# Kernel tuning notes

Measured on AMD Instinct MI355X. Metric: run time of the kernel, lower is better.

The kernel has to match this reference:

```python
import jax, jax.numpy as jnp
import numpy as np

N, E = 65536, 524288
IN, H, OUT, L = 128, 128, 64, 2
TAU = 0.5
NUM_HEAT = 5

def _lin(x, w, b):
    return x @ w + b

def _aggregate(x, row, col, ew, n):
    # gather-mul-scatter neighbor mean: out[r] = sum_e ew[e]*x[col[e]] / max(deg[r],1)
    msg = x[col] * ew[:, None]
    out = jax.ops.segment_sum(msg, row, num_segments=n)
    deg = jnp.clip(jax.ops.segment_sum(ew, row, num_segments=n), 1.0, None)
    return out / deg[:, None]

def setup_inputs() -> dict:
    key = jax.random.key(0)
    k = jax.random.split(key, 24)
    def w(i, shape):
        fan_in = shape[-2]
        return (jax.random.normal(k[i], shape, dtype=jnp.float32) / np.sqrt(fan_in)).astype(jnp.float32)
    # every node appears in row at least once -> deg > 0 everywhere
    row = jax.random.permutation(k[0], jnp.arange(E, dtype=jnp.int32) % N)
    col = jax.random.randint(k[1], (E,), 0, N, dtype=jnp.int32)
    return {
        "x": jax.random.normal(k[2], (N, IN), dtype=jnp.float32),
        "edge_index": jnp.stack([row, col]),
        "timestamps": jax.random.uniform(k[3], (N, 1), dtype=jnp.float32),
        "edge_weight": jax.random.uniform(k[4], (E,), dtype=jnp.float32) + 0.1,
        "prev_embedding": jnp.zeros((1, H), dtype=jnp.float32),
        "gumbel": -jnp.log(-jnp.log(jax.random.uniform(k[5], (5,), minval=1e-6, maxval=1.0))),
        "ctrl_w1": w(6, (8 + H, 128)), "ctrl_b1": jnp.zeros((128,), jnp.float32),
        "ctrl_w2": w(7, (128, 5)), "ctrl_b2": jnp.zeros((5,), jnp.float32),
        "mode_bias": jnp.zeros((5,), jnp.float32),
        "att_w1": w(8, (2 * H, 64)), "att_b1": jnp.zeros((64,), jnp.float32),
        "att_w2": w(9, (64, 1)), "att_b2": jnp.zeros((1,), jnp.float32),
        "heat_kernels": jnp.linspace(0.1, 2.0, NUM_HEAT, dtype=jnp.float32),
        "tg_w": w(10, (H + 1, H)), "tg_b": jnp.zeros((H,), jnp.float32),
        "scale_weights": jnp.ones((3,), jnp.float32),
        "spatial_w": w(11, (L, H, H)), "spatial_b": jnp.zeros((L, H), jnp.float32),
        "temporal_w": w(12, (L, H, H)), "temporal_b": jnp.zeros((L, H), jnp.float32),
        "attention_w": w(13, (L, H, H)), "attention_b": jnp.zeros((L, H), jnp.float32),
        "diffusion_w": w(14, (L, H, H)), "diffusion_b": jnp.zeros((L, H), jnp.float32),
        "hier_w": w(15, (L, H, H)), "hier_b": jnp.zeros((L, H), jnp.float32),
        "out_w1": w(16, (H, H // 2)), "out_b1": jnp.zeros((H // 2,), jnp.float32),
        "out_w2": w(17, (H // 2, OUT)), "out_b2": jnp.zeros((OUT,), jnp.float32),
    }

def reference(x, edge_index, timestamps, edge_weight, prev_embedding, gumbel,
              ctrl_w1, ctrl_b1, ctrl_w2, ctrl_b2, mode_bias,
              att_w1, att_b1, att_w2, att_b2, heat_kernels, tg_w, tg_b, scale_weights,
              spatial_w, spatial_b, temporal_w, temporal_b, attention_w, attention_b,
              diffusion_w, diffusion_b, hier_w, hier_b,
              out_w1, out_b1, out_w2, out_b2):
    row, col = edge_index[0], edge_index[1]
    n, e = x.shape[0], row.shape[0]
    ones_e = jnp.ones((e,), x.dtype)
    deg = jax.ops.segment_sum(ones_e, row, num_segments=n)
    # stats are .item()-detached in torch -> stop_gradient here; torch std is unbiased (ddof=1)
    stats = jax.lax.stop_gradient(jnp.stack([
        jnp.asarray(n / 1000.0, x.dtype), jnp.asarray(e / max(n, 1), x.dtype),
        jnp.std(deg, ddof=1), (deg == 0).astype(x.dtype).mean(),
        x.mean(), jnp.std(x, ddof=1), edge_weight.mean(),
        jnp.asarray(e / (n * n), x.dtype)]))
    quality = prev_embedding.mean(axis=0)
    logits = _lin(jax.nn.relu(_lin(jnp.concatenate([stats, quality]), ctrl_w1, ctrl_b1)), ctrl_w2, ctrl_b2) + mode_bias
    probs = jax.nn.softmax((logits + gumbel) / TAU)  # soft gumbel-softmax, noise precomputed

    # spatial pass
    xs = x
    for i in range(L):
        xs = jax.nn.relu(_aggregate(_lin(xs, spatial_w[i], spatial_b[i]), row, col, edge_weight, n))
    # temporal pass
    xt = x
    for i in range(L):
        h = _lin(xt, temporal_w[i], temporal_b[i])
        gate = jax.nn.sigmoid(_lin(jnp.concatenate([h, timestamps], axis=-1), tg_w, tg_b))
        agg = _aggregate(h, row, col, ones_e, n)
        xt = jax.nn.relu(gate * h + (1 - gate) * agg)
    # attention pass (global softmax over all edges, as in torch dim=0)
    xa = x
    for i in range(L):
        h = _lin(xa, attention_w[i], attention_b[i])
        score = _lin(jax.nn.relu(_lin(jnp.concatenate([h[row], h[col]], axis=-1), att_w1, att_b1)), att_w2, att_b2)[:, 0]
        attn = jax.nn.softmax(score)
        xa = jax.nn.relu(jax.ops.segment_sum(h[col] * attn[:, None], row, num_segments=n))
    # diffusion pass
    dis = jnp.clip(deg ** -0.5, 1e-8, None)
    norm = dis[row] * dis[col]
    xd = x
    for i in range(L):
        h = _lin(xd, diffusion_w[i], diffusion_b[i])
        outs = []
        for j in range(NUM_HEAT):
            t = heat_kernels[j]
            hk = jax.ops.segment_sum(h[col] * norm[:, None], row, num_segments=n)
            h = (1 - t) * h + t * hk
            outs.append(h)
        xd = jax.nn.relu(jnp.mean(jnp.stack(outs), axis=0))
    # hierarchical pass
    xh = x
    wsc = jax.nn.softmax(scale_weights)
    for i in range(L):
        h = _lin(xh, hier_w[i], hier_b[i])
        h1 = _aggregate(h, row, col, ones_e, n)
        h2 = _aggregate(h1, row, col, ones_e, n)
        h3 = _aggregate(h2, row, col, ones_e, n)
        xh = jax.nn.relu(wsc[0] * h1 + wsc[1] * h2 + wsc[2] * h3)

    # torch skips branches with probs<=0.001 (zero contribution)
    g = jnp.where(probs > 0.001, probs, 0.0)
    xsum = g[0] * xs + g[1] * xt + g[2] * xa + g[3] * xd + g[4] * xh
    return _lin(jax.nn.relu(_lin(xsum, out_w1, out_b1)), out_w2, out_b2)
```

## Files before the change

kernel.cpp:

```cpp
#include <hip/hip_runtime.h>
#include <hip/hip_bf16.h>
#include <math.h>


#define NN   65536
#define EE   524288
#define HH   128
#define NF   (NN*HH)
#define PAD  136

typedef __hip_bfloat16 bf16;
typedef unsigned int   u32;
typedef unsigned short u16;
typedef __attribute__((ext_vector_type(8))) short s8v;
typedef __attribute__((ext_vector_type(4))) float f32x4;

__device__ __forceinline__ float b2f(bf16 v){ return __bfloat162float(v); }
__device__ __forceinline__ bf16  f2b(float v){ return __float2bfloat16(v); }
__device__ __forceinline__ float lo2f(u32 u){ return __uint_as_float(u<<16); }
__device__ __forceinline__ float hi2f(u32 u){ return __uint_as_float(u & 0xffff0000u); }
__device__ __forceinline__ u32 pack2(float a, float b){
  bf16 ba = f2b(a), bb = f2b(b);
  u16 ua = *reinterpret_cast<u16*>(&ba);
  u16 ub = *reinterpret_cast<u16*>(&bb);
  return ((u32)ub<<16) | (u32)ua;
}
__device__ __forceinline__ unsigned fenc(float f){ unsigned u=__float_as_uint(f); return (u&0x80000000u)?~u:(u|0x80000000u); }
__device__ __forceinline__ float fdec(unsigned u){ return __uint_as_float((u&0x80000000u)?(u&0x7fffffffu):~u); }
__device__ __forceinline__ float ldf(const void* p, size_t i, int isbf){
  return isbf ? b2f(((const bf16*)p)[i]) : ((const float*)p)[i];
}


__global__ void k_fill(float* p, float v, int n){
  int i = blockIdx.x*blockDim.x + threadIdx.x;
  if (i < n) p[i] = v;
}
__global__ void k_sentinel(u16* p, int n){
  int i = blockIdx.x*blockDim.x + threadIdx.x;
  if (i < n) p[i] = 0x4640;
}
__global__ void k_init(float* scal){
  int i = threadIdx.x;
  if (i < 32) scal[i] = 0.f;
  if (i == 6) ((unsigned*)scal)[6] = 0x007fffffu;
  if (i == 8) ((unsigned*)scal)[8] = 0x80000000u;
}
__global__ void k_init_attn(float* scal){
  if (threadIdx.x==0){ ((unsigned*)scal)[6] = 0x007fffffu; scal[7] = 0.f; }
}

__global__ void k_probe(const uint4* __restrict__ ew4, float* scal){
  __shared__ float red[4];
  int i = blockIdx.x*256 + threadIdx.x;
  uint4 v = ew4[i];
  float m = 0.f;
  u32 ws[4] = {v.x, v.y, v.z, v.w};
  #pragma unroll
  for (int q=0;q<4;++q){
    float a = lo2f(ws[q]), b = hi2f(ws[q]);
    a = isfinite(a) ? fabsf(a) : 1e30f;
    b = isfinite(b) ? fabsf(b) : 1e30f;
    m = fmaxf(m, fmaxf(a,b));
  }
  for (int o=32;o;o>>=1) m = fmaxf(m, __shfl_down(m, o, 64));
  if ((threadIdx.x&63)==0) red[threadIdx.x>>6] = m;
  __syncthreads();
  if (threadIdx.x==0){
    m = fmaxf(fmaxf(red[0],red[1]), fmaxf(red[2],red[3]));
    atomicMax((unsigned*)scal + 8, fenc(m));
  }
}
__global__ void k_flag(float* scal){
  if (threadIdx.x==0){
    float m = fdec(((const unsigned*)scal)[8]);
    scal[9] = (m < 64.f) ? 1.f : 0.f;
  }
}

__global__ void k_csr(const int* __restrict__ row, const int* __restrict__ col,
                      const void* __restrict__ ew, int* cnt,
                      int* __restrict__ colS, float* __restrict__ wS, const float* scal){
  int isbf = scal[9] > 0.5f;
  int e = blockIdx.x*blockDim.x + threadIdx.x;
  int r = row[e];
  float w = ldf(ew, e, isbf);
  int slot = atomicAdd(&cnt[r], 1) & 7;
  int p = r*8 + slot;
  colS[p] = col[e];
  wS[p] = w;
}

__global__ void k_node(const int* __restrict__ cnt, const float* __restrict__ wS,
                       float* deg, float* degw, float* dis, float* bsc, float* scal){
  __shared__ float red[4][4];
  int i = blockIdx.x*256 + threadIdx.x;
  float dd = (float)cnt[i];
  const float4* w4 = (const float4*)(wS + i*8);
  float4 wa = w4[0], wb = w4[1];
  float s = wa.x+wa.y+wa.z+wa.w + wb.x+wb.y+wb.z+wb.w;
  deg[i] = dd; degw[i] = s;
  dis[i] = (dd>0.f) ? (1.f/sqrtf(dd)) : 1e8f;
  bsc[i] = fminf(s, 1.f);
// ... 165 lines not shown

__global__ __launch_bounds__(256) void k_mgemm(
    const void* __restrict__ Aext, const bf16* __restrict__ Ab,
    const float* __restrict__ Af, int K,
    const bf16* __restrict__ Wt, const void* __restrict__ bias, int Boff, int Nout,
    bf16* __restrict__ outB, float* __restrict__ outF, void* __restrict__ outE,
    const void* __restrict__ ts, const float* __restrict__ rbs,
    const bf16* __restrict__ eh, const bf16* __restrict__ eg,
    int act, int bbf, const float* __restrict__ fl){
  __shared__ bf16 sA[64*PAD];
  __shared__ bf16 sW[128*PAD];
  int flA = fl[0] > 0.5f;
  int tid = threadIdx.x;
  int rowBase = blockIdx.x*64;
  {
    int tot = (Nout*PAD)/8;
    const uint4* src = (const uint4*)Wt;
    uint4* dst = (uint4*)sW;
    for (int i = tid; i < tot; i += 256) dst[i] = src[i];
  }
  {
    int kc = K/8;
    for (int i = tid; i < 64*kc; i += 256){
      int m = i/kc, c = i - m*kc;
      size_t gi = (size_t)(rowBase+m)*K + (size_t)c*8;
      uint4 v;
      if (Ab) v = *(const uint4*)(Ab+gi);
      else if (Af){
        float4 f0 = *(const float4*)(Af+gi);
        float4 f1 = *(const float4*)(Af+gi+4);
        v.x=pack2(f0.x,f0.y); v.y=pack2(f0.z,f0.w); v.z=pack2(f1.x,f1.y); v.w=pack2(f1.z,f1.w);
      } else if (flA) v = *(const uint4*)((const bf16*)Aext+gi);
      else {
        const float* Ax = (const float*)Aext;
        float4 f0 = *(const float4*)(Ax+gi);
        float4 f1 = *(const float4*)(Ax+gi+4);
        v.x=pack2(f0.x,f0.y); v.y=pack2(f0.z,f0.w); v.z=pack2(f1.x,f1.y); v.w=pack2(f1.z,f1.w);
      }
      *(uint4*)&sA[m*PAD + c*8] = v;
    }
  }
  __syncthreads();
  int wave = tid>>6, lane = tid&63;
  int m0 = wave*16;
  int l15 = lane&15, quad = lane>>4;
  int ntiles = Nout>>4, ksteps = K>>5;
  f32x4 acc[8];
  #pragma unroll
  for (int t=0;t<8;++t) acc[t] = (f32x4){0.f,0.f,0.f,0.f};
  for (int ks=0; ks<ksteps; ++ks){
    int kb = ks*32 + quad*8;
    s8v af = *(const s8v*)&sA[(m0 + l15)*PAD + kb];
    for (int t=0;t<ntiles;++t){
      s8v bfr = *(const s8v*)&sW[(t*16 + l15)*PAD + kb];
      acc[t] = __builtin_amdgcn_mfma_f32_16x16x32_bf16(af, bfr, acc[t], 0, 0, 0);
    }
  }
  int isbfB = bbf || flA;
  for (int t=0;t<ntiles;++t){
    int colN = t*16 + l15;
    float bv = isbfB ? b2f(((const bf16*)bias)[Boff+colN]) : ((const float*)bias)[Boff+colN];
    float w128 = ts ? b2f(sW[colN*PAD + K]) : 0.f;
    #pragma unroll
    for (int r=0;r<4;++r){
      int rowG = rowBase + m0 + quad*4 + r;
      float bscale = rbs ? rbs[rowG] : 1.f;
      float v = acc[t][r] + bv*bscale;
      if (ts) v += (flA ? b2f(((const bf16*)ts)[rowG]) : ((const float*)ts)[rowG]) * w128;
      if (eh){
        float gp = b2f(eg[(size_t)rowG*Nout + colN]);
        float sg = 1.f/(1.f+expf(-gp));
        v = sg*b2f(eh[(size_t)rowG*Nout + colN]) + (1.f-sg)*v;
      }
      if (act) v = fmaxf(v, 0.f);
      size_t oi = (size_t)rowG*Nout + colN;
      if (outB) outB[oi] = f2b(v);
      else if (outF) outF[oi] = v;
      else if (flA) ((bf16*)outE)[oi] = f2b(v);
      else ((float*)outE)[oi] = v;
    }
  }
}

__global__ __launch_bounds__(256) void k_mgemm_mix(
    const bf16* __restrict__ s0, const bf16* __restrict__ s1,
    const bf16* __restrict__ s2, const bf16* __restrict__ s3,
    const bf16* __restrict__ s4, int nsrc, int cbase,
    const bf16* __restrict__ Wt, const void* __restrict__ bias, int Boff,
    bf16* __restrict__ outB, const float* __restrict__ fl,
    const float* __restrict__ scal){
  __shared__ bf16 sA[64*PAD];
  __shared__ bf16 sW[128*PAD];
  int isbf = fl[0] > 0.5f;
  int tid = threadIdx.x;
  int rowBase = blockIdx.x*64;
  {
    int tot = (128*PAD)/8;
    const uint4* src = (const uint4*)Wt;
    uint4* dst = (uint4*)sW;
    for (int i = tid; i < tot; i += 256) dst[i] = src[i];
  }
  float c0 = scal[cbase], c1 = scal[cbase+1], c2 = scal[cbase+2];
  float c3 = (nsrc>3) ? scal[cbase+3] : 0.f;
  for (int i = tid; i < 64*16; i += 256){
    int m = i>>4, cc = i&15;
    size_t gi = (size_t)(rowBase+m)*128 + (size_t)cc*8;
    float v[8];
    {
      uint4 a = *(const uint4*)(s0+gi); u32 aw[4]={a.x,a.y,a.z,a.w};
      #pragma unroll
      for (int q=0;q<4;++q){ v[2*q]=c0*lo2f(aw[q]); v[2*q+1]=c0*hi2f(aw[q]); }
    }
    {
      uint4 a = *(const uint4*)(s1+gi); u32 aw[4]={a.x,a.y,a.z,a.w};
      #pragma unroll
      for (int q=0;q<4;++q){ v[2*q]+=c1*lo2f(aw[q]); v[2*q+1]+=c1*hi2f(aw[q]); }
    }
    {
      uint4 a = *(const uint4*)(s2+gi); u32 aw[4]={a.x,a.y,a.z,a.w};
      #pragma unroll
      for (int q=0;q<4;++q){ v[2*q]+=c2*lo2f(aw[q]); v[2*q+1]+=c2*hi2f(aw[q]); }
    }
    if (nsrc > 3){
      uint4 a = *(const uint4*)(s3+gi); u32 aw[4]={a.x,a.y,a.z,a.w};
      #pragma unroll
      for (int q=0;q<4;++q){ v[2*q]+=c3*lo2f(aw[q]); v[2*q+1]+=c3*hi2f(aw[q]); }
      uint4 b = *(const uint4*)(s4+gi); u32 bw[4]={b.x,b.y,b.z,b.w};
      #pragma unroll
      for (int q=0;q<4;++q){ v[2*q]+=lo2f(bw[q]); v[2*q+1]+=hi2f(bw[q]); }
    }
    uint4 ov; ov.x=pack2(v[0],v[1]); ov.y=pack2(v[2],v[3]);
    ov.z=pack2(v[4],v[5]); ov.w=pack2(v[6],v[7]);
    *(uint4*)&sA[m*PAD + cc*8] = ov;
  }
  __syncthreads();
  int wave = tid>>6, lane = tid&63;
  int m0 = wave*16, l15 = lane&15, quad = lane>>4;
  f32x4 acc[8];
  #pragma unroll
  for (int t=0;t<8;++t) acc[t] = (f32x4){0.f,0.f,0.f,0.f};
  for (int ks=0; ks<4; ++ks){
    int kb = ks*32 + quad*8;
    s8v af = *(const s8v*)&sA[(m0 + l15)*PAD + kb];
    #pragma unroll
    for (int t=0;t<8;++t){
      s8v bfr = *(const s8v*)&sW[(t*16 + l15)*PAD + kb];
      acc[t] = __builtin_amdgcn_mfma_f32_16x16x32_bf16(af, bfr, acc[t], 0, 0, 0);
    }
  }
  #pragma unroll
  for (int t=0;t<8;++t){
    int colN = t*16 + l15;
    float bv = isbf ? b2f(((const bf16*)bias)[Boff+colN]) : ((const float*)bias)[Boff+colN];
    #pragma unroll
    for (int r=0;r<4;++r){
      int rowG = rowBase + m0 + quad*4 + r;
      float v = fmaxf(acc[t][r] + bv, 0.f);
      outB[(size_t)rowG*128 + colN] = f2b(v);
    }
  }
}

template<int MODE>
__global__ __launch_bounds__(256) void g_agg4(
    const bf16* __restrict__ Hin, bf16* __restrict__ out, bf16* __restrict__ hout,
    bf16* __restrict__ acc2,
    const int* __restrict__ colS, const float* __restrict__ wS,
    const float* __restrict__ nrmS, const float* __restrict__ escS,
    const float* __restrict__ degv, const float* __restrict__ dw2,
    const void* __restrict__ heat, int hidx, int flags, int gidx,
    const float* __restrict__ scal){
  int tid = threadIdx.x;
  int r = blockIdx.x*16 + (tid>>4);
  int lf = tid & 15;
  int base = r*8;
  int4 ci0 = *(const int4*)(colS + base);
  int4 ci1 = *(const int4*)(colS + base + 4);
  int cs[8] = {ci0.x,ci0.y,ci0.z,ci0.w,ci1.x,ci1.y,ci1.z,ci1.w};
  float w[8];
  if (MODE==0 || MODE==2 || MODE==3){
    const float* wp = (MODE==0) ? wS : (MODE==2 ? escS : nrmS);
    float4 a = *(const float4*)(wp+base), b4 = *(const float4*)(wp+base+4);
    w[0]=a.x; w[1]=a.y; w[2]=a.z; w[3]=a.w;
    w[4]=b4.x; w[5]=b4.y; w[6]=b4.z; w[7]=b4.w;
    if (MODE==2){
      float inv = 1.f/fmaxf(scal[7], 1e-30f);
      #pragma unroll
      for (int q=0;q<8;++q) w[q] *= inv;
    }
  }
  float wb[8];
  if (MODE==8){
    float4 a = *(const float4*)(wS+base), b4 = *(const float4*)(wS+base+4);
    wb[0]=a.x; wb[1]=a.y; wb[2]=a.z; wb[3]=a.w;
    wb[4]=b4.x; wb[5]=b4.y; wb[6]=b4.z; wb[7]=b4.w;
  }
  float acc[8], accB[8];
  #pragma unroll
  for (int q=0;q<8;++q){ acc[q]=0.f; if (MODE==8) accB[q]=0.f; }
  const bf16* hbase = Hin + lf*8;
  #pragma unroll
  for (int s=0;s<8;++s){
    uint4 hv = *(const uint4*)(hbase + ((size_t)cs[s]<<7));
    u32 hw[4] = {hv.x,hv.y,hv.z,hv.w};
    #pragma unroll
    for (int q=0;q<4;++q){
      float lo = lo2f(hw[q]), hi = hi2f(hw[q]);
      if (MODE==0 || MODE==2 || MODE==3){
        acc[2*q]   += w[s]*lo;
        acc[2*q+1] += w[s]*hi;
      } else {
        acc[2*q] += lo; acc[2*q+1] += hi;
        if (MODE==8){ accB[2*q] += wb[s]*lo; accB[2*q+1] += wb[s]*hi; }
      }
    }
  }
  size_t rb = (size_t)r*HH + lf*8;
  float val[8], val2[8];
  if (MODE==0){
    float id = 1.f/fmaxf(degv[r], 1.f);
    #pragma unroll
    for (int q=0;q<8;++q) val[q] = fmaxf(acc[q]*id, 0.f);
  } else if (MODE==1){
    float id = 1.f/fmaxf(degv[r], 1.f);
    uint4 gv = *(const uint4*)(out + rb);
    uint4 hv = *(const uint4*)(Hin + rb);
    u32 gw[4]={gv.x,gv.y,gv.z,gv.w}, hw[4]={hv.x,hv.y,hv.z,hv.w};
    #pragma unroll
    for (int q=0;q<4;++q){
      float s0 = 1.f/(1.f+expf(-lo2f(gw[q])));
      float s1 = 1.f/(1.f+expf(-hi2f(gw[q])));
      val[2*q]   = fmaxf(s0*lo2f(hw[q]) + (1.f-s0)*acc[2*q]*id,   0.f);
      val[2*q+1] = fmaxf(s1*hi2f(hw[q]) + (1.f-s1)*acc[2*q+1]*id, 0.f);
    }
  } else if (MODE==2){
    #pragma unroll
    for (int q=0;q<8;++q) val[q] = fmaxf(acc[q], 0.f);
  } else if (MODE==3){
    uint4 hv = *(const uint4*)(Hin + rb);
    u32 hw[4]={hv.x,hv.y,hv.z,hv.w};
    float tt = ldf(heat, hidx, scal[9]>0.5f);
    float hn[8];
    #pragma unroll
    for (int q=0;q<4;++q){
      hn[2*q]   = (1.f-tt)*lo2f(hw[q]) + tt*acc[2*q];
      hn[2*q+1] = (1.f-tt)*hi2f(hw[q]) + tt*acc[2*q+1];
    }
    if (!(flags&2)){
      uint4 ov; ov.x=pack2(hn[0],hn[1]); ov.y=pack2(hn[2],hn[3]);
      ov.z=pack2(hn[4],hn[5]); ov.w=pack2(hn[6],hn[7]);
      *(uint4*)(hout + rb) = ov;
    }
    if (flags&1){
      #pragma unroll
      for (int q=0;q<8;++q) val[q] = hn[q];
    } else {
      uint4 pv = *(const uint4*)(out + rb);
      u32 pw[4]={pv.x,pv.y,pv.z,pv.w};
      #pragma unroll
      for (int q=0;q<4;++q){
        val[2*q]   = lo2f(pw[q]) + hn[2*q];
        val[2*q+1] = hi2f(pw[q]) + hn[2*q+1];
      }
    }
    if (flags&2){
      #pragma unroll
      for (int q=0;q<8;++q) val[q] = fmaxf(0.2f*val[q], 0.f);
    }
  } else if (MODE==4){
    float id = 1.f/fmaxf(degv[r], 1.f);
    #pragma unroll
    for (int q=0;q<8;++q) val[q] = acc[q]*id;
  } else if (MODE==5){
    float id = 1.f/fmaxf(degv[r], 1.f);
    float w0=scal[15], w1=scal[16], w2=scal[17];
    uint4 a1 = *(const uint4*)(hout + rb);
    uint4 a2 = *(const uint4*)(Hin + rb);
    u32 x1[4]={a1.x,a1.y,a1.z,a1.w}, x2[4]={a2.x,a2.y,a2.z,a2.w};
    #pragma unroll
    for (int q=0;q<4;++q){
      val[2*q]   = fmaxf(w0*lo2f(x1[q]) + w1*lo2f(x2[q]) + w2*acc[2*q]*id,   0.f);
      val[2*q+1] = fmaxf(w0*hi2f(x1[q]) + w1*hi2f(x2[q]) + w2*acc[2*q+1]*id, 0.f);
    }
  } else {
    float id  = 1.f/fmaxf(degv[r], 1.f);
    float idw = 1.f/fmaxf(dw2[r], 1.f);
    #pragma unroll
    for (int q=0;q<8;++q){ val[q] = acc[q]*id; val2[q] = accB[q]*idw; }
  }
  if (!(flags&16)){
    uint4 ov; ov.x=pack2(val[0],val[1]); ov.y=pack2(val[2],val[3]);
    ov.z=pack2(val[4],val[5]); ov.w=pack2(val[6],val[7]);
    *(uint4*)(out + rb) = ov;
  }
  if (MODE==8){
    uint4 ov; ov.x=pack2(val2[0],val2[1]); ov.y=pack2(val2[2],val2[3]);
    ov.z=pack2(val2[4],val2[5]); ov.w=pack2(val2[6],val2[7]);
    *(uint4*)(hout + rb) = ov;
  }
  if (flags&4){
    float g = scal[10+gidx];
    float av[8];
    if (flags&8){
      #pragma unroll
      for (int q=0;q<8;++q) av[q] = g*val[q];
    } else {
      uint4 bv = *(const uint4*)(acc2 + rb);
      u32 bw[4]={bv.x,bv.y,bv.z,bv.w};
      #pragma unroll
      for (int q=0;q<4;++q){
        av[2*q]   = lo2f(bw[q]) + g*val[2*q];
        av[2*q+1] = hi2f(bw[q]) + g*val[2*q+1];
      }
    }
    uint4 sv; sv.x=pack2(av[0],av[1]); sv.y=pack2(av[2],av[3]);
    sv.z=pack2(av[4],av[5]); sv.w=pack2(av[6],av[7]);
    *(uint4*)(acc2 + rb) = sv;
  }
}

__global__ __launch_bounds__(256) void k_edge_score4(
    const float* __restrict__ Huv, const int* __restrict__ colS,
    const void* __restrict__ aw2, const void* __restrict__ ab2,
    float* __restrict__ escS, const float* __restrict__ fl){
  int isbf = fl[0] > 0.5f;
  int tid = threadIdx.x;
  int r = blockIdx.x*4 + (tid>>6);
  int lane = tid & 63;
  int ef = lane>>3, ff = lane&7;
  int p = r*8 + ef;
  int c = colS[p];
  const float* up = Huv + (size_t)r*128 + ff*8;
  const float* vp = Huv + (size_t)c*128 + 64 + ff*8;
  float4 u0 = *(const float4*)up,     u1 = *(const float4*)(up+4);
  float4 v0 = *(const float4*)vp,     v1 = *(const float4*)(vp+4);
  float w2v[8];
  if (isbf){
    const bf16* a2 = (const bf16*)aw2 + ff*8;
    uint4 t4 = *(const uint4*)a2;
    u32 tw[4]={t4.x,t4.y,t4.z,t4.w};
    #pragma unroll
    for (int q=0;q<4;++q){ w2v[2*q]=lo2f(tw[q]); w2v[2*q+1]=hi2f(tw[q]); }
  } else {
    const float* a2 = (const float*)aw2 + ff*8;
    float4 f0 = *(const float4*)a2, f1 = *(const float4*)(a2+4);
    w2v[0]=f0.x; w2v[1]=f0.y; w2v[2]=f0.z; w2v[3]=f0.w;
    w2v[4]=f1.x; w2v[5]=f1.y; w2v[6]=f1.z; w2v[7]=f1.w;
  }
  float s = 0.f;
  s += fmaxf(u0.x+v0.x,0.f)*w2v[0];
  s += fmaxf(u0.y+v0.y,0.f)*w2v[1];
  s += fmaxf(u0.z+v0.z,0.f)*w2v[2];
  s += fmaxf(u0.w+v0.w,0.f)*w2v[3];
  s += fmaxf(u1.x+v1.x,0.f)*w2v[4];
  s += fmaxf(u1.y+v1.y,0.f)*w2v[5];
  s += fmaxf(u1.z+v1.z,0.f)*w2v[6];
  s += fmaxf(u1.w+v1.w,0.f)*w2v[7];
  s += __shfl_xor(s, 1, 64);
  s += __shfl_xor(s, 2, 64);
  s += __shfl_xor(s, 4, 64);
  if (ff == 0) escS[p] = s + ldf(ab2, 0, isbf);
}

__global__ void k_score_max(const float4* __restrict__ sc4, float* scal){
  __shared__ float red[4];
  float m = -1e30f;
  for (int i = blockIdx.x*256 + threadIdx.x; i < EE/4; i += 256*256){
    float4 v = sc4[i];
    m = fmaxf(fmaxf(m, fmaxf(v.x,v.y)), fmaxf(v.z,v.w));
  }
  for (int o=32;o;o>>=1) m = fmaxf(m, __shfl_down(m, o, 64));
  if ((threadIdx.x&63)==0) red[threadIdx.x>>6] = m;
  __syncthreads();
  if (threadIdx.x==0){
    m = fmaxf(fmaxf(red[0],red[1]), fmaxf(red[2],red[3]));
    atomicMax((unsigned*)scal + 6, fenc(m));
  }
}
__global__ void k_score_exp(float4* __restrict__ sc4, float* scal){
  __shared__ float red[4];
  float mx = fdec(((const unsigned*)scal)[6]);
  float s = 0.f;
  for (int i = blockIdx.x*256 + threadIdx.x; i < EE/4; i += 256*256){
    float4 v = sc4[i];
    v.x = expf(v.x-mx); v.y = expf(v.y-mx); v.z = expf(v.z-mx); v.w = expf(v.w-mx);
    sc4[i] = v;
    s += v.x+v.y+v.z+v.w;
  }
  for (int o=32;o;o>>=1) s += __shfl_down(s, o, 64);
  if ((threadIdx.x&63)==0) red[threadIdx.x>>6] = s;
  __syncthreads();
  if (threadIdx.x==0) atomicAdd(&scal[7], red[0]+red[1]+red[2]+red[3]);
}

extern "C" void kernel_launch(void* const* d_in, const int* in_sizes, int n_in,
                              void* d_out, int out_size, void* d_ws, size_t ws_size,
                              hipStream_t stream){
  (void)in_sizes; (void)n_in;
  const void* x    = d_in[0];
  const int*  ei   = (const int*)d_in[1];
  const void* tsv  = d_in[2];
  const void* ew   = d_in[3];
  const void* prev = d_in[4];
  const void* gum  = d_in[5];
  const void* cw1  = d_in[6];
  const void* cb1  = d_in[7];
  const void* cw2  = d_in[8];
  const void* cb2  = d_in[9];
  const void* mbias= d_in[10];
  const void* aw1  = d_in[11];
  const void* ab1  = d_in[12];
  const void* aw2  = d_in[13];
  const void* ab2  = d_in[14];
  const void* heat = d_in[15];
  const void* tgw  = d_in[16];
  const void* tgb  = d_in[17];
  const void* scw  = d_in[18];
  const void* spw  = d_in[19];
  const void* spb  = d_in[20];
  const void* tww  = d_in[21];
  const void* twb  = d_in[22];
  const void* atw  = d_in[23];
  const void* atb  = d_in[24];
  const void* diw  = d_in[25];
  const void* dib  = d_in[26];
  const void* hiw  = d_in[27];
  const void* hib  = d_in[28];
  const void* ow1  = d_in[29];
  const void* ob1  = d_in[30];
  const void* ow2  = d_in[31];
  const void* ob2  = d_in[32];
  const int* row = ei, *col = ei + EE;

  const size_t SL = (size_t)NF;
  const size_t WT10 = 10*128*PAD, WTE = 128*PAD, WTO = 64*PAD;

  bf16* Hb   = (bf16*)d_ws;
  bf16* Hb2  = Hb + SL;
  bf16* B1   = Hb2 + SL;
  bf16* B2   = B1 + SL;
  float* escS= (float*)(B2 + SL);
  int*   colS= (int*)(escS + EE);
  float* wS  = (float*)(colS + EE);
  int*   cnt = (int*)(wS + EE);
  float* deg = (float*)(cnt + NN);
  float* degw= deg + NN;
  float* dis = degw + NN;
  bf16* wt_l = (bf16*)(dis + NN);
  bf16* wt_tg= wt_l + WT10;
  bf16* wt_ct= wt_tg + WTE;
  bf16* wt_o1= wt_ct + WTE;
  bf16* wt_o2= wt_o1 + WTO;
  bf16* bcat = wt_o2 + WTO;
  float* scal= (float*)(bcat + 128);
  const float* fl = scal + 9;
  float* nrmS = scal + 32;
  float* bsc  = nrmS + EE;
  bf16* VD = (bf16*)(bsc + NN);
  bf16* VE = VD + SL;
  bf16* VF = VE + SL;
  float* Huv = (float*)Hb2;

  size_t need_old = (size_t)((char*)VD - (char*)d_ws);
  size_t need_new = (size_t)((char*)(VF + SL) - (char*)d_ws);
  if (ws_size < need_old){
    k_sentinel<<<(out_size+255)/256,256,0,stream>>>((u16*)d_out, out_size);
    return;
  }
  bool KRY = ws_size >= need_new;

  const int TB = 256;
  const int GAG = NN/16;
  const int GES = NN/4;
  const int GMM = NN/64;

  k_init<<<1,64,0,stream>>>(scal);
  k_probe<<<EE/8/TB,TB,0,stream>>>((const uint4*)ew, scal);
  k_flag<<<1,64,0,stream>>>(scal);
  k_wt10<<<(10*128*PAD+TB-1)/TB,TB,0,stream>>>(spw, tww, atw, diw, hiw, wt_l, fl);
  k_wt<<<(128*PAD+TB-1)/TB,TB,0,stream>>>(tgw, 129, 128, wt_tg, fl);
  k_wt<<<(64*PAD+TB-1)/TB,TB,0,stream>>>(ow1, 128, 64, wt_o1, fl);
  k_wt<<<(64*PAD+TB-1)/TB,TB,0,stream>>>(ow2, 64, 64, wt_o2, fl);
  k_wt_cat<<<(128*PAD+TB-1)/TB,TB,0,stream>>>(aw1, ab1, wt_ct, bcat, fl);
  k_fill<<<NN/TB,TB,0,stream>>>((float*)cnt, 0.f, NN);
  k_csr<<<EE/TB,TB,0,stream>>>(row, col, ew, cnt, colS, wS, scal);
  k_node<<<NN/TB,TB,0,stream>>>(cnt, wS, deg, degw, dis, bsc, scal);
  k_nrm<<<EE/TB,TB,0,stream>>>(colS, dis, nrmS);
  k_x_stats<<<512,TB,0,stream>>>(x, scal);
  k_ctrl<<<1,128,0,stream>>>(scal, prev, cw1, cb1, cw2, cb2, mbias, gum, scw, heat);

  auto mgemm = [&](const void* Aext, const bf16* Ab, const float* Af, int K,
                   const bf16* Wt, const void* B, int Boff, int Nout,
                   bf16* oB, float* oF, void* oE, const void* tsp,
                   const float* rbs, const bf16* eh, const bf16* eg,
                   int act, int bbf){
    k_mgemm<<<GMM, TB, 0, stream>>>(Aext, Ab, Af, K, Wt, B, Boff, Nout,
                                    oB, oF, oE, tsp, rbs, eh, eg, act, bbf, fl);
  };
  auto agg = [&](int mode, const bf16* Hin, bf16* out, bf16* ho, bf16* ac2,
                 int flags, int gidx, const float* dv, const float* dw2, int hidx){
    switch(mode){
      case 0: g_agg4<0><<<GAG,TB,0,stream>>>(Hin,out,ho,ac2,colS,wS,nrmS,escS,dv,dw2,heat,hidx,flags,gidx,scal); break;
      case 1: g_agg4<1><<<GAG,TB,0,stream>>>(Hin,out,ho,ac2,colS,wS,nrmS,escS,dv,dw2,heat,hidx,flags,gidx,scal); break;
      case 2: g_agg4<2><<<GAG,TB,0,stream>>>(Hin,out,ho,ac2,colS,wS,nrmS,escS,dv,dw2,heat,hidx,flags,gidx,scal); break;
      case 3: g_agg4<3><<<GAG,TB,0,stream>>>(Hin,out,ho,ac2,colS,wS,nrmS,escS,dv,dw2,heat,hidx,flags,gidx,scal); break;
      case 4: g_agg4<4><<<GAG,TB,0,stream>>>(Hin,out,ho,ac2,colS,wS,nrmS,escS,dv,dw2,heat,hidx,flags,gidx,scal); break;
      case 5: g_agg4<5><<<GAG,TB,0,stream>>>(Hin,out,ho,ac2,colS,wS,nrmS,escS,dv,dw2,heat,hidx,flags,gidx,scal); break;
      default:g_agg4<8><<<GAG,TB,0,stream>>>(Hin,out,ho,ac2,colS,wS,nrmS,escS,dv,dw2,heat,hidx,flags,gidx,scal); break;
    }
  };

  if (KRY){
    k_tobf<<<NF/8/TB,TB,0,stream>>>(x, Hb2, fl);
    agg(8, Hb2, VD, Hb, nullptr, 0, 0, deg, degw, 0);
    mgemm(nullptr, Hb, nullptr, 128, wt_l, spb, 0, 128,
          B1, nullptr, nullptr, nullptr, bsc, nullptr, nullptr, 1, 0);
    mgemm(nullptr, B1, nullptr, 128, wt_l + WTE, spb, 128, 128,
          Hb, nullptr, nullptr, nullptr, nullptr, nullptr, nullptr, 0, 0);
    agg(0, Hb, B1, nullptr, B2, 4|8, 0, degw, nullptr, 0);
    agg(4, VD, VE, nullptr, nullptr, 0, 0, deg, nullptr, 0);
    agg(4, VE, VF, nullptr, nullptr, 0, 0, deg, nullptr, 0);
    agg(4, VF, Hb, nullptr, B1, 4|8, 18, deg, nullptr, 0);
    agg(4, Hb, Hb, nullptr, B1, 4|16, 19, deg, nullptr, 0);
    k_mgemm_mix<<<GMM,TB,0,stream>>>(Hb2, VD, VE, VF, B1, 5, 24,
                                     wt_l + 6*WTE, dib, 0, B1, fl, scal);
    mgemm(nullptr, B1, nullptr, 128, wt_l + 7*WTE, dib, 128, 128,
          Hb, nullptr, nullptr, nullptr, nullptr, nullptr, nullptr, 0, 0);
    {
      bf16* hin = Hb; bf16* hot = Hb2;
      for (int j=0;j<5;++j){
        int flags = (j==0?1:0) | (j==4?2:0) | (j==4?4:0);
        agg(3, hin, B1, hot, B2, flags, 3, deg, nullptr, j);
        bf16* t = hin; hin = hot; hot = t;
      }
    }
    mgemm(x, nullptr, nullptr, 128, wt_l + 2*WTE, twb, 0, 128,
          Hb, nullptr, nullptr, nullptr, nullptr, nullptr, nullptr, 0, 0);
    mgemm(nullptr, Hb, nullptr, 128, wt_tg, tgb, 0, 128,
          B1, nullptr, nullptr, tsv, nullptr, nullptr, nullptr, 0, 0);
    mgemm(nullptr, VD, nullptr, 128, wt_l + 2*WTE, twb, 0, 128,
          B1, nullptr, nullptr, nullptr, nullptr, Hb, B1, 1, 0);
    mgemm(nullptr, B1, nullptr, 128, wt_l + 3*WTE, twb, 128, 128,
          Hb, nullptr, nullptr, nullptr, nullptr, nullptr, nullptr, 0, 0);
    mgemm(nullptr, Hb, nullptr, 128, wt_tg, tgb, 0, 128,
          B1, nullptr, nullptr, tsv, nullptr, nullptr, nullptr, 0, 0);
    agg(1, Hb, B1, nullptr, B2, 4, 1, deg, nullptr, 0);
    k_mgemm_mix<<<GMM,TB,0,stream>>>(VD, VE, VF, nullptr, nullptr, 3, 15,
                                     wt_l + 8*WTE, hib, 0, B1, fl, scal);
    mgemm(nullptr, B1, nullptr, 128, wt_l + 9*WTE, hib, 128, 128,
          Hb, nullptr, nullptr, nullptr, nullptr, nullptr, nullptr, 0, 0);
    agg(4, Hb,  Hb2, nullptr, nullptr, 0, 0, deg, nullptr, 0);
    agg(4, Hb2, Hb,  nullptr, nullptr, 0, 0, deg, nullptr, 0);
    agg(5, Hb,  B1,  Hb2,     B2, 4, 4, deg, nullptr, 0);
    for (int i=0;i<2;++i){
      mgemm(i?nullptr:x, i?B1:nullptr, nullptr, 128, wt_l + (size_t)(4+i)*WTE, atb, i*128, 128,
            Hb, nullptr, nullptr, nullptr, nullptr, nullptr, nullptr, 0, 0);
      mgemm(nullptr, Hb, nullptr, 128, wt_ct, bcat, 0, 128,
            nullptr, Huv, nullptr, nullptr, nullptr, nullptr, nullptr, 0, 1);
      k_edge_score4<<<GES,TB,0,stream>>>(Huv, colS, aw2, ab2, escS, fl);
      k_init_attn<<<1,64,0,stream>>>(scal);
      k_score_max<<<256,TB,0,stream>>>((const float4*)escS, scal);
      k_score_exp<<<256,TB,0,stream>>>((float4*)escS, scal);
      agg(2, Hb, B1, nullptr, B2, i?4:0, 2, deg, nullptr, 0);
    }
  } else {
    for (int i=0;i<2;++i){
      mgemm(i?nullptr:x, i?B1:nullptr, nullptr, 128, wt_l + (size_t)i*WTE, spb, i*128, 128,
            Hb, nullptr, nullptr, nullptr, nullptr, nullptr, nullptr, 0, 0);
      agg(0, Hb, B1, nullptr, B2, i?(4|8):0, 0, degw, nullptr, 0);
    }
    for (int i=0;i<2;++i){
      mgemm(i?nullptr:x, i?B1:nullptr, nullptr, 128, wt_l + (size_t)(2+i)*WTE, twb, i*128, 128,
            Hb, nullptr, nullptr, nullptr, nullptr, nullptr, nullptr, 0, 0);
      mgemm(nullptr, Hb, nullptr, 128, wt_tg, tgb, 0, 128,
            B1, nullptr, nullptr, tsv, nullptr, nullptr, nullptr, 0, 0);
      agg(1, Hb, B1, nullptr, B2, i?4:0, 1, deg, nullptr, 0);
    }
    for (int i=0;i<2;++i){
      mgemm(i?nullptr:x, i?B1:nullptr, nullptr, 128, wt_l + (size_t)(4+i)*WTE, atb, i*128, 128,
            Hb, nullptr, nullptr, nullptr, nullptr, nullptr, nullptr, 0, 0);
      mgemm(nullptr, Hb, nullptr, 128, wt_ct, bcat, 0, 128,
            nullptr, Huv, nullptr, nullptr, nullptr, nullptr, nullptr, 0, 1);
      k_edge_score4<<<GES,TB,0,stream>>>(Huv, colS, aw2, ab2, escS, fl);
      k_init_attn<<<1,64,0,stream>>>(scal);
      k_score_max<<<256,TB,0,stream>>>((const float4*)escS, scal);
      k_score_exp<<<256,TB,0,stream>>>((float4*)escS, scal);
      agg(2, Hb, B1, nullptr, B2, i?4:0, 2, deg, nullptr, 0);
    }
    for (int i=0;i<2;++i){
      mgemm(i?nullptr:x, i?B1:nullptr, nullptr, 128, wt_l + (size_t)(6+i)*WTE, dib, i*128, 128,
            Hb, nullptr, nullptr, nullptr, nullptr, nullptr, nullptr, 0, 0);
      bf16* hin = Hb; bf16* hot = Hb2;
      for (int j=0;j<5;++j){
        int flags = (j==0?1:0) | (j==4?2:0) | ((i==1&&j==4)?4:0);
        agg(3, hin, B1, hot, B2, flags, 3, deg, nullptr, j);
        bf16* t = hin; hin = hot; hot = t;
      }
    }
    for (int i=0;i<2;++i){
      mgemm(i?nullptr:x, i?B1:nullptr, nullptr, 128, wt_l + (size_t)(8+i)*WTE, hib, i*128, 128,
            Hb, nullptr, nullptr, nullptr, nullptr, nullptr, nullptr, 0, 0);
      agg(4, Hb,  Hb2, nullptr, nullptr, 0, 0, deg, nullptr, 0);
      agg(4, Hb2, Hb,  nullptr, nullptr, 0, 0, deg, nullptr, 0);
      agg(5, Hb,  B1,  Hb2,     B2, i?4:0, 4, deg, nullptr, 0);
    }
  }

  mgemm(nullptr, B2, nullptr, 128, wt_o1, ob1, 0, 64,
        nullptr, (float*)Hb, nullptr, nullptr, nullptr, nullptr, nullptr, 1, 0);
  mgemm(nullptr, nullptr, (float*)Hb, 64, wt_o2, ob2, 0, 64,
        nullptr, nullptr, d_out, nullptr, nullptr, nullptr, nullptr, 0, 0);
}
```

Measured before the change: 1.234 ms.

## Fuse back-to-back GEMM pairs into single kernels keeping intermediate in LDS

```diff
diff --git a/kernel.cpp b/kernel.cpp
--- a/kernel.cpp
+++ b/kernel.cpp
@@ -19,6 +19,7 @@
 __device__ __forceinline__ bf16  f2b(float v){ return __float2bfloat16(v); }
 __device__ __forceinline__ float lo2f(u32 u){ return __uint_as_float(u<<16); }
 __device__ __forceinline__ float hi2f(u32 u){ return __uint_as_float(u & 0xffff0000u); }
+__device__ __forceinline__ float hi2r(u32 u){ return __uint_as_float(u); }
 __device__ __forceinline__ u32 pack2(float a, float b){
   bf16 ba = f2b(a), bb = f2b(b);
   u16 ua = *reinterpret_cast<u16*>(&ba);
@@ -350,11 +351,112 @@
   }
 }
 
-__global__ __launch_bounds__(256) void k_mgemm_mix(
+__global__ __launch_bounds__(256) void k_mg2(
+    const void* __restrict__ Aext, const bf16* __restrict__ Ab,
+    const bf16* __restrict__ W1t, const void* __restrict__ b1, int b1off, int N1,
+    int act1, const float* __restrict__ rbs, bf16* __restrict__ hOut,
+    const bf16* __restrict__ W2t, const void* __restrict__ b2, int b2off, int bbf2,
+    int N2, const void* __restrict__ ts,
+    bf16* __restrict__ out2B, void* __restrict__ out2E,
+    const float* __restrict__ fl){
+  __shared__ bf16 sA[64*PAD];
+  __shared__ bf16 sW[128*PAD];
+  int flA = fl[0] > 0.5f;
+  int tid = threadIdx.x;
+  int rowBase = blockIdx.x*64;
+  {
+    int tot = (N1*PAD)/8;
+    const uint4* src = (const uint4*)W1t;
+    uint4* dst = (uint4*)sW;
+    for (int i = tid; i < tot; i += 256) dst[i] = src[i];
+  }
+  {
+    for (int i = tid; i < 64*16; i += 256){
+      int m = i>>4, c = i&15;
+      size_t gi = (size_t)(rowBase+m)*128 + (size_t)c*8;
+      uint4 v;
+      if (Ab) v = *(const uint4*)(Ab+gi);
+      else if (flA) v = *(const uint4*)((const bf16*)Aext+gi);
+      else {
+        const float* Ax = (const float*)Aext;
+        float4 f0 = *(const float4*)(Ax+gi);
+        float4 f1 = *(const float4*)(Ax+gi+4);
+        v.x=pack2(f0.x,f0.y); v.y=pack2(f0.z,f0.w); v.z=pack2(f1.x,f1.y); v.w=pack2(f1.z,f1.w);
+      }
+      *(uint4*)&sA[m*PAD + c*8] = v;
+    }
+  }
+  __syncthreads();
+  int wave = tid>>6, lane = tid&63;
+  int m0 = wave*16, l15 = lane&15, quad = lane>>4;
+  int nt1 = N1>>4;
+  f32x4 acc[8];
+  #pragma unroll
+  for (int t=0;t<8;++t) acc[t] = (f32x4){0.f,0.f,0.f,0.f};
+  for (int ks=0; ks<4; ++ks){
+    int kb = ks*32 + quad*8;
+    s8v af = *(const s8v*)&sA[(m0 + l15)*PAD + kb];
+    for (int t=0;t<nt1;++t){
+      s8v bfr = *(const s8v*)&sW[(t*16 + l15)*PAD + kb];
+      acc[t] = __builtin_amdgcn_mfma_f32_16x16x32_bf16(af, bfr, acc[t], 0, 0, 0);
+    }
+  }
+  for (int t=0;t<nt1;++t){
+    int colN = t*16 + l15;
+    float bv = ldf(b1, b1off+colN, flA);
+    #pragma unroll
+    for (int r=0;r<4;++r){
+      int rowL = m0 + quad*4 + r;
+      float v = acc[t][r] + bv*(rbs ? rbs[rowBase+rowL] : 1.f);
+      if (act1) v = fmaxf(v, 0.f);
+      bf16 hb = f2b(v);
+      sA[rowL*PAD + colN] = hb;
+      if (hOut) hOut[(size_t)(rowBase+rowL)*N1 + colN] = hb;
+    }
+  }
+  __syncthreads();
+  {
+    int tot = (N2*PAD)/8;
+    const uint4* src = (const uint4*)W2t;
+    uint4* dst = (uint4*)sW;
+    for (int i = tid; i < tot; i += 256) dst[i] = src[i];
+  }
+  __syncthreads();
+  int nt2 = N2>>4, ks2 = N1>>5;
+  #pragma unroll
+  for (int t=0;t<8;++t) acc[t] = (f32x4){0.f,0.f,0.f,0.f};
+  for (int ks=0; ks<ks2; ++ks){
+    int kb = ks*32 + quad*8;
+    s8v af = *(const s8v*)&sA[(m0 + l15)*PAD + kb];
+    for (int t=0;t<nt2;++t){
+      s8v bfr = *(const s8v*)&sW[(t*16 + l15)*PAD + kb];
+      acc[t] = __builtin_amdgcn_mfma_f32_16x16x32_bf16(af, bfr, acc[t], 0, 0, 0);
+    }
+  }
+  int isbf2 = bbf2 || flA;
+  for (int t=0;t<nt2;++t){
+    int colN = t*16 + l15;
+    float bv = isbf2 ? b2f(((const bf16*)b2)[b2off+colN]) : ((const float*)b2)[b2off+colN];
+    float w128 = ts ? b2f(sW[colN*PAD + N1]) : 0.f;
+    #pragma unroll
+    for (int r=0;r<4;++r){
+      int rowG = rowBase + m0 + quad*4 + r;
+      float v = acc[t][r] + bv;
+      if (ts) v += (flA ? b2f(((const bf16*)ts)[rowG]) : ((const float*)ts)[rowG]) * w128;
+      size_t oi = (size_t)rowG*N2 + colN;
+      if (out2B) out2B[oi] = f2b(v);
+      else if (flA) ((bf16*)out2E)[oi] = f2b(v);
+      else ((float*)out2E)[oi] = v;
+    }
+  }
+}
+
+__global__ __launch_bounds__(256) void k_mix2(
     const bf16* __restrict__ s0, const bf16* __restrict__ s1,
     const bf16* __restrict__ s2, const bf16* __restrict__ s3,
     const bf16* __restrict__ s4, int nsrc, int cbase,
-    const bf16* __restrict__ Wt, const void* __restrict__ bias, int Boff,
+    const bf16* __restrict__ W1t, const void* __restrict__ b1, int b1off,
+    const bf16* __restrict__ W2t, const void* __restrict__ b2, int b2off,
     bf16* __restrict__ outB, const float* __restrict__ fl,
     const float* __restrict__ scal){
   __shared__ bf16 sA[64*PAD];
@@ -364,7 +466,7 @@
   int rowBase = blockIdx.x*64;
   {
     int tot = (128*PAD)/8;
-    const uint4* src = (const uint4*)Wt;
+    const uint4* src = (const uint4*)W1t;
     uint4* dst = (uint4*)sW;
     for (int i = tid; i < tot; i += 256) dst[i] = src[i];
   }
@@ -419,12 +521,41 @@
   #pragma unroll
   for (int t=0;t<8;++t){
     int colN = t*16 + l15;
-    float bv = isbf ? b2f(((const bf16*)bias)[Boff+colN]) : ((const float*)bias)[Boff+colN];
+    float bv = ldf(b1, b1off+colN, isbf);
+    #pragma unroll
+    for (int r=0;r<4;++r){
+      int rowL = m0 + quad*4 + r;
+      float v = fmaxf(acc[t][r] + bv, 0.f);
+      sA[rowL*PAD + colN] = f2b(v);
+    }
+  }
+  __syncthreads();
+  {
+    int tot = (128*PAD)/8;
+    const uint4* src = (const uint4*)W2t;
+    uint4* dst = (uint4*)sW;
+    for (int i = tid; i < tot; i += 256) dst[i] = src[i];
+  }
+  __syncthreads();
+  #pragma unroll
+  for (int t=0;t<8;++t) acc[t] = (f32x4){0.f,0.f,0.f,0.f};
+  for (int ks=0; ks<4; ++ks){
+    int kb = ks*32 + quad*8;
+    s8v af = *(const s8v*)&sA[(m0 + l15)*PAD + kb];
+    #pragma unroll
+    for (int t=0;t<8;++t){
+      s8v bfr = *(const s8v*)&sW[(t*16 + l15)*PAD + kb];
+      acc[t] = __builtin_amdgcn_mfma_f32_16x16x32_bf16(af, bfr, acc[t], 0, 0, 0);
+    }
+  }
+  #pragma unroll
+  for (int t=0;t<8;++t){
+    int colN = t*16 + l15;
+    float bv = ldf(b2, b2off+colN, isbf);
     #pragma unroll
     for (int r=0;r<4;++r){
       int rowG = rowBase + m0 + quad*4 + r;
-      float v = fmaxf(acc[t][r] + bv, 0.f);
-      outB[(size_t)rowG*128 + colN] = f2b(v);
+      outB[(size_t)rowG*128 + colN] = f2b(acc[t][r] + bv);
     }
   }
 }
@@ -473,7 +604,7 @@
     u32 hw[4] = {hv.x,hv.y,hv.z,hv.w};
     #pragma unroll
     for (int q=0;q<4;++q){
-      float lo = lo2f(hw[q]), hi = hi2f(hw[q]);
+      float lo = lo2f(hw[q]), hi = hi2r(hw[q]);
       if (MODE==0 || MODE==2 || MODE==3){
         acc[2*q]   += w[s]*lo;
         acc[2*q+1] += w[s]*hi;
@@ -588,9 +719,9 @@
 }
 
 __global__ __launch_bounds__(256) void k_edge_score4(
-    const float* __restrict__ Huv, const int* __restrict__ colS,
+    const void* __restrict__ Huv, const int* __restrict__ colS,
     const void* __restrict__ aw2, const void* __restrict__ ab2,
-    float* __restrict__ escS, const float* __restrict__ fl){
+    float* __restrict__ escS, int hbf, const float* __restrict__ fl){
   int isbf = fl[0] > 0.5f;
   int tid = threadIdx.x;
   int r = blockIdx.x*4 + (tid>>6);
@@ -598,10 +729,25 @@
   int ef = lane>>3, ff = lane&7;
   int p = r*8 + ef;
   int c = colS[p];
-  const float* up = Huv + (size_t)r*128 + ff*8;
-  const float* vp = Huv + (size_t)c*128 + 64 + ff*8;
-  float4 u0 = *(const float4*)up,     u1 = *(const float4*)(up+4);
-  float4 v0 = *(const float4*)vp,     v1 = *(const float4*)(vp+4);
+  float u[8], v[8];
+  if (hbf){
+    const bf16* up = (const bf16*)Huv + (size_t)r*128 + ff*8;
+    const bf16* vp = (const bf16*)Huv + (size_t)c*128 + 64 + ff*8;
+    uint4 uu = *(const uint4*)up, vv = *(const uint4*)vp;
+    u32 a[4]={uu.x,uu.y,uu.z,uu.w}, b[4]={vv.x,vv.y,vv.z,vv.w};
+    #pragma unroll
+    for (int q=0;q<4;++q){
+      u[2*q]=lo2f(a[q]); u[2*q+1]=hi2f(a[q]);
+      v[2*q]=lo2f(b[q]); v[2*q+1]=hi2f(b[q]);
+    }
+  } else {
+    const float* up = (const float*)Huv + (size_t)r*128 + ff*8;
+    const float* vp = (const float*)Huv + (size_t)c*128 + 64 + ff*8;
+    float4 u0 = *(const float4*)up, u1 = *(const float4*)(up+4);
+    float4 v0 = *(const float4*)vp, v1 = *(const float4*)(vp+4);
+    u[0]=u0.x;u[1]=u0.y;u[2]=u0.z;u[3]=u0.w;u[4]=u1.x;u[5]=u1.y;u[6]=u1.z;u[7]=u1.w;
+    v[0]=v0.x;v[1]=v0.y;v[2]=v0.z;v[3]=v0.w;v[4]=v1.x;v[5]=v1.y;v[6]=v1.z;v[7]=v1.w;
+  }
   float w2v[8];
   if (isbf){
     const bf16* a2 = (const bf16*)aw2 + ff*8;
@@ -616,14 +762,8 @@
     w2v[4]=f1.x; w2v[5]=f1.y; w2v[6]=f1.z; w2v[7]=f1.w;
   }
   float s = 0.f;
-  s += fmaxf(u0.x+v0.x,0.f)*w2v[0];
-  s += fmaxf(u0.y+v0.y,0.f)*w2v[1];
-  s += fmaxf(u0.z+v0.z,0.f)*w2v[2];
-  s += fmaxf(u0.w+v0.w,0.f)*w2v[3];
-  s += fmaxf(u1.x+v1.x,0.f)*w2v[4];
-  s += fmaxf(u1.y+v1.y,0.f)*w2v[5];
-  s += fmaxf(u1.z+v1.z,0.f)*w2v[6];
-  s += fmaxf(u1.w+v1.w,0.f)*w2v[7];
+  #pragma unroll
+  for (int q=0;q<8;++q) s += fmaxf(u[q]+v[q],0.f)*w2v[q];
   s += __shfl_xor(s, 1, 64);
   s += __shfl_xor(s, 2, 64);
   s += __shfl_xor(s, 4, 64);
@@ -765,6 +905,14 @@
     k_mgemm<<<GMM, TB, 0, stream>>>(Aext, Ab, Af, K, Wt, B, Boff, Nout,
                                     oB, oF, oE, tsp, rbs, eh, eg, act, bbf, fl);
   };
+  auto mg2 = [&](const void* Aext, const bf16* Ab,
+                 const bf16* W1, const void* b1, int b1off, int N1, int act1,
+                 const float* rbs, bf16* hOut,
+                 const bf16* W2, const void* b2, int b2off, int bbf2, int N2,
+                 const void* tsp, bf16* o2B, void* o2E){
+    k_mg2<<<GMM, TB, 0, stream>>>(Aext, Ab, W1, b1, b1off, N1, act1, rbs, hOut,
+                                  W2, b2, b2off, bbf2, N2, tsp, o2B, o2E, fl);
+  };
   auto agg = [&](int mode, const bf16* Hin, bf16* out, bf16* ho, bf16* ac2,
                  int flags, int gidx, const float* dv, const float* dw2, int hidx){
     switch(mode){
@@ -781,19 +929,16 @@
   if (KRY){
     k_tobf<<<NF/8/TB,TB,0,stream>>>(x, Hb2, fl);
     agg(8, Hb2, VD, Hb, nullptr, 0, 0, deg, degw, 0);
-    mgemm(nullptr, Hb, nullptr, 128, wt_l, spb, 0, 128,
-          B1, nullptr, nullptr, nullptr, bsc, nullptr, nullptr, 1, 0);
-    mgemm(nullptr, B1, nullptr, 128, wt_l + WTE, spb, 128, 128,
-          Hb, nullptr, nullptr, nullptr, nullptr, nullptr, nullptr, 0, 0);
+    mg2(nullptr, Hb, wt_l, spb, 0, 128, 1, bsc, nullptr,
+        wt_l + WTE, spb, 128, 0, 128, nullptr, Hb, nullptr);
     agg(0, Hb, B1, nullptr, B2, 4|8, 0, degw, nullptr, 0);
     agg(4, VD, VE, nullptr, nullptr, 0, 0, deg, nullptr, 0);
     agg(4, VE, VF, nullptr, nullptr, 0, 0, deg, nullptr, 0);
     agg(4, VF, Hb, nullptr, B1, 4|8, 18, deg, nullptr, 0);
     agg(4, Hb, Hb, nullptr, B1, 4|16, 19, deg, nullptr, 0);
-    k_mgemm_mix<<<GMM,TB,0,stream>>>(Hb2, VD, VE, VF, B1, 5, 24,
-                                     wt_l + 6*WTE, dib, 0, B1, fl, scal);
-    mgemm(nullptr, B1, nullptr, 128, wt_l + 7*WTE, dib, 128, 128,
-          Hb, nullptr, nullptr, nullptr, nullptr, nullptr, nullptr, 0, 0);
+    k_mix2<<<GMM,TB,0,stream>>>(Hb2, VD, VE, VF, B1, 5, 24,
+                                wt_l + 6*WTE, dib, 0,
+                                wt_l + 7*WTE, dib, 128, Hb, fl, scal);
     {
       bf16* hin = Hb; bf16* hot = Hb2;
       for (int j=0;j<5;++j){
@@ -802,35 +947,30 @@
         bf16* t = hin; hin = hot; hot = t;
       }
     }
-    mgemm(x, nullptr, nullptr, 128, wt_l + 2*WTE, twb, 0, 128,
-          Hb, nullptr, nullptr, nullptr, nullptr, nullptr, nullptr, 0, 0);
-    mgemm(nullptr, Hb, nullptr, 128, wt_tg, tgb, 0, 128,
-          B1, nullptr, nullptr, tsv, nullptr, nullptr, nullptr, 0, 0);
+    mg2(x, nullptr, wt_l + 2*WTE, twb, 0, 128, 0, nullptr, Hb,
+        wt_tg, tgb, 0, 0, 128, tsv, B1, nullptr);
     mgemm(nullptr, VD, nullptr, 128, wt_l + 2*WTE, twb, 0, 128,
           B1, nullptr, nullptr, nullptr, nullptr, Hb, B1, 1, 0);
-    mgemm(nullptr, B1, nullptr, 128, wt_l + 3*WTE, twb, 128, 128,
-          Hb, nullptr, nullptr, nullptr, nullptr, nullptr, nullptr, 0, 0);
-    mgemm(nullptr, Hb, nullptr, 128, wt_tg, tgb, 0, 128,
-          B1, nullptr, nullptr, tsv, nullptr, nullptr, nullptr, 0, 0);
+    mg2(nullptr, B1, wt_l + 3*WTE, twb, 128, 128, 0, nullptr, Hb,
+        wt_tg, tgb, 0, 0, 128, tsv, B1, nullptr);
     agg(1, Hb, B1, nullptr, B2, 4, 1, deg, nullptr, 0);
-    k_mgemm_mix<<<GMM,TB,0,stream>>>(VD, VE, VF, nullptr, nullptr, 3, 15,
-                                     wt_l + 8*WTE, hib, 0, B1, fl, scal);
-    mgemm(nullptr, B1, nullptr, 128, wt_l + 9*WTE, hib, 128, 128,
-          Hb, nullptr, nullptr, nullptr, nullptr, nullptr, nullptr, 0, 0);
+    k_mix2<<<GMM,TB,0,stream>>>(VD, VE, VF, VD, VD, 3, 15,
+                                wt_l + 8*WTE, hib, 0,
+                                wt_l + 9*WTE, hib, 128, Hb, fl, scal);
     agg(4, Hb,  Hb2, nullptr, nullptr, 0, 0, deg, nullptr, 0);
     agg(4, Hb2, Hb,  nullptr, nullptr, 0, 0, deg, nullptr, 0);
     agg(5, Hb,  B1,  Hb2,     B2, 4, 4, deg, nullptr, 0);
     for (int i=0;i<2;++i){
-      mgemm(i?nullptr:x, i?B1:nullptr, nullptr, 128, wt_l + (size_t)(4+i)*WTE, atb, i*128, 128,
-            Hb, nullptr, nullptr, nullptr, nullptr, nullptr, nullptr, 0, 0);
-      mgemm(nullptr, Hb, nullptr, 128, wt_ct, bcat, 0, 128,
-            nullptr, Huv, nullptr, nullptr, nullptr, nullptr, nullptr, 0, 1);
-      k_edge_score4<<<GES,TB,0,stream>>>(Huv, colS, aw2, ab2, escS, fl);
+      mg2(i?nullptr:x, i?B1:nullptr, wt_l + (size_t)(4+i)*WTE, atb, i*128, 128, 0,
+          nullptr, Hb, wt_ct, bcat, 0, 1, 128, nullptr, Hb2, nullptr);
+      k_edge_score4<<<GES,TB,0,stream>>>(Hb2, colS, aw2, ab2, escS, 1, fl);
       k_init_attn<<<1,64,0,stream>>>(scal);
       k_score_max<<<256,TB,0,stream>>>((const float4*)escS, scal);
       k_score_exp<<<256,TB,0,stream>>>((float4*)escS, scal);
       agg(2, Hb, B1, nullptr, B2, i?4:0, 2, deg, nullptr, 0);
     }
+    mg2(nullptr, B2, wt_o1, ob1, 0, 64, 1, nullptr, nullptr,
+        wt_o2, ob2, 0, 0, 64, nullptr, nullptr, d_out);
   } else {
     for (int i=0;i<2;++i){
       mgemm(i?nullptr:x, i?B1:nullptr, nullptr, 128, wt_l + (size_t)i*WTE, spb, i*128, 128,
@@ -849,7 +989,7 @@
             Hb, nullptr, nullptr, nullptr, nullptr, nullptr, nullptr, 0, 0);
       mgemm(nullptr, Hb, nullptr, 128, wt_ct, bcat, 0, 128,
             nullptr, Huv, nullptr, nullptr, nullptr, nullptr, nullptr, 0, 1);
-      k_edge_score4<<<GES,TB,0,stream>>>(Huv, colS, aw2, ab2, escS, fl);
+      k_edge_score4<<<GES,TB,0,stream>>>(Huv, colS, aw2, ab2, escS, 0, fl);
       k_init_attn<<<1,64,0,stream>>>(scal);
       k_score_max<<<256,TB,0,stream>>>((const float4*)escS, scal);
       k_score_exp<<<256,TB,0,stream>>>((float4*)escS, scal);
@@ -872,10 +1012,9 @@
       agg(4, Hb2, Hb,  nullptr, nullptr, 0, 0, deg, nullptr, 0);
       agg(5, Hb,  B1,  Hb2,     B2, i?4:0, 4, deg, nullptr, 0);
     }
-  }
-
-  mgemm(nullptr, B2, nullptr, 128, wt_o1, ob1, 0, 64,
-        nullptr, (float*)Hb, nullptr, nullptr, nullptr, nullptr, nullptr, 1, 0);
-  mgemm(nullptr, nullptr, (float*)Hb, 64, wt_o2, ob2, 0, 64,
-        nullptr, nullptr, d_out, nullptr, nullptr, nullptr, nullptr, 0, 0);
-}
+    mgemm(nullptr, B2, nullptr, 128, wt_o1, ob1, 0, 64,
+          nullptr, (float*)Hb, nullptr, nullptr, nullptr, nullptr, nullptr, 1, 0);
+    mgemm(nullptr, nullptr, (float*)Hb, 64, wt_o2, ob2, 0, 64,
+          nullptr, nullptr, d_out, nullptr, nullptr, nullptr, nullptr, 0, 0);
+  }
+}
```

Result: faster. 1.091 ms (-11.6%).
